# Kernel tuning notes

Hardware: AMD Instinct MI355X
Metric: run time of the kernel (lower is better)

Reference implementation:

```python
import jax, jax.numpy as jnp
import numpy as np

N_NODES = 46080   # 512 graphs x 90 nodes
NPG = 90          # nodes per graph (AAL atlas)
G = 512           # number of graphs
E = 737280        # edges (degree 16)
IN_DIM = 90
H = 64            # hidden_channels
K = 70            # sort-pool k


def setup_inputs() -> dict:
    key = jax.random.key(0)
    ks = jax.random.split(key, 12)
    x = jax.random.normal(ks[0], (N_NODES, IN_DIM), dtype=jnp.float32)
    # intra-graph random edges: src/dst within each graph's 90-node block
    gidx = jnp.repeat(jnp.arange(G, dtype=jnp.int64), E // G) * NPG
    src = jax.random.randint(ks[1], (E,), 0, NPG, dtype=jnp.int64) + gidx
    dst = jax.random.randint(ks[2], (E,), 0, NPG, dtype=jnp.int64) + gidx
    edge_index = jnp.stack([src, dst])
    edge_weight = jax.random.uniform(ks[3], (E,), dtype=jnp.float32)
    batch = jnp.repeat(jnp.arange(G, dtype=jnp.int64), NPG)
    s1 = 1.0 / np.sqrt(IN_DIM)
    s2 = 1.0 / np.sqrt(H)
    sk = 1.0 / np.sqrt(H * K)
    W1 = jax.random.uniform(ks[4], (IN_DIM, H), jnp.float32, -s1, s1)
    b1 = jnp.zeros((H,), jnp.float32)
    W2 = jax.random.uniform(ks[5], (H, H), jnp.float32, -s2, s2)
    b2 = jnp.zeros((H,), jnp.float32)
    lw1 = jax.random.uniform(ks[6], (H * K, H), jnp.float32, -sk, sk)
    lb1 = jax.random.uniform(ks[7], (H,), jnp.float32, -sk, sk)
    lw2 = jax.random.uniform(ks[8], (H, 1), jnp.float32, -s2, s2)
    lb2 = jax.random.uniform(ks[9], (1,), jnp.float32, -s2, s2)
    return {"x": x, "edge_index": edge_index, "edge_weight": edge_weight,
            "batch": batch, "W1": W1, "b1": b1, "W2": W2, "b2": b2,
            "lw1": lw1, "lb1": lb1, "lw2": lw2, "lb2": lb2}


def _gcn_conv(x, W, b, src, dst, ew, n):
    # PyG GCNConv: add self-loops (weight 1), symmetric normalization,
    # message = norm * (x @ W)[src], scatter-add to dst, add bias.
    xw = x @ W
    loop = jnp.arange(n)
    src_f = jnp.concatenate([src, loop])
    dst_f = jnp.concatenate([dst, loop])
    ew_f = jnp.concatenate([ew, jnp.ones((n,), x.dtype)])
    deg = jax.ops.segment_sum(ew_f, dst_f, num_segments=n)
    dinv = jnp.where(deg > 0, jax.lax.rsqrt(jnp.maximum(deg, 1e-12)), 0.0)
    norm = dinv[src_f] * ew_f * dinv[dst_f]
    msg = xw[src_f] * norm[:, None]          # [E+n, H] irregular gather
    out = jax.ops.segment_sum(msg, dst_f, num_segments=n)
    return out + b


def reference(x, edge_index, edge_weight, batch, W1, b1, W2, b2, lw1, lb1, lw2, lb2):
    src, dst = edge_index[0], edge_index[1]
    h1 = _gcn_conv(x, W1, b1, src, dst, edge_weight, N_NODES)
    x_train = h1
    h = jax.nn.relu(h1)
    h2 = _gcn_conv(h, W2, b2, src, dst, edge_weight, N_NODES)
    # global_sort_pool: per graph, sort nodes descending by last channel, keep top K.
    # batch is contiguous with NPG nodes/graph, so a reshape is exact.
    hg = h2.reshape(G, NPG, H)
    order = jnp.argsort(-hg[:, :, -1], axis=1)          # [G, NPG] descending
    hs = jnp.take_along_axis(hg, order[:, :, None], axis=1)
    pooled = hs[:, :K, :].reshape(G, K * H)
    # F.dropout(p=0.5, training=False) -> identity at inference
    z = pooled @ lw1 + lb1
    z = z @ lw2 + lb2
    out = jax.nn.sigmoid(z).squeeze(-1)                  # [G]
    return out, x_train
```

## Files before the change

kernel.cpp:

```cpp
#include <hip/hip_runtime.h>


#define NG      512
#define NPG     90
#define EPG     1440
#define IN_DIM  90
#define HD      64
#define KP      70
#define E_TOT   (NG*EPG)

#define WEFF_OFF   0
#define EPACK_OFF  4608
#define RS_OFF     (EPACK_OFF + NG*EPG)
#define D2_OFF     (RS_OFF + NG*96)
#define HW2_OFF    (D2_OFF + NG*96)

__global__ __launch_bounds__(256) void k0_csr(
    const int* __restrict__ ei, const float* __restrict__ ew,
    const float* __restrict__ lw1, const float* __restrict__ lb1,
    const float* __restrict__ lw2, const float* __restrict__ lb2,
    float* __restrict__ ws)
{
    __shared__ float s_deg[NPG];
    __shared__ int   s_indeg[NPG];
    __shared__ int   s_rowstart[NPG+1];
    __shared__ int   s_cursor[NPG];

    const int g = blockIdx.x, t = threadIdx.x;
    const int ebase = g*EPG, nbase = g*NPG;

    if (t < NPG) { s_deg[t] = 1.0f; s_indeg[t] = 0; }
    __syncthreads();
    for (int e = t; e < EPG; e += 256) {
        int d = ei[E_TOT + ebase + e] - nbase;
        atomicAdd(&s_deg[d], ew[ebase + e]);
        atomicAdd(&s_indeg[d], 1);
    }
    __syncthreads();
    if (t < NPG) s_deg[t] = rsqrtf(fmaxf(s_deg[t], 1e-12f));
    if (t <= NPG) {
        int acc = 0;
        for (int i = 0; i < t; ++i) acc += s_indeg[i];
        s_rowstart[t] = acc;
        if (t < NPG) s_cursor[t] = acc;
    }
    __syncthreads();

    unsigned* epk = (unsigned*)ws + EPACK_OFF + g*EPG;
    for (int e = t; e < EPG; e += 256) {
        int s = ei[ebase + e] - nbase;
        int d = ei[E_TOT + ebase + e] - nbase;
        float nrm = s_deg[s] * ew[ebase + e] * s_deg[d];
        int pos = atomicAdd(&s_cursor[d], 1);
        epk[pos] = (__float_as_uint(nrm) & ~127u) | (unsigned)s;
    }
    if (t <= NPG) ((int*)ws)[RS_OFF + g*96 + t] = s_rowstart[t];
    if (t < NPG)  ws[D2_OFF + g*96 + t] = s_deg[t]*s_deg[t];

    int i = g*256 + t;
    if (g < 18) {
        if (i < KP*HD) {
            const float4* row = (const float4*)(lw1 + (size_t)i*HD);
            const float4* w   = (const float4*)lw2;
            float s = 0.f;
            #pragma unroll
            for (int j4 = 0; j4 < HD/4; ++j4) {
                float4 r = row[j4], v = w[j4];
                s += r.x*v.x + r.y*v.y + r.z*v.z + r.w*v.w;
            }
            ws[WEFF_OFF + i] = s;
        } else if (i == KP*HD) {
            float s = lb2[0];
            for (int jj = 0; jj < HD; ++jj) s += lb1[jj]*lw2[jj];
            ws[WEFF_OFF + KP*HD] = s;
        }
    }
}

__global__ __launch_bounds__(256) void k1_gemm1(
    const float* __restrict__ x, const float* __restrict__ W1,
    float* __restrict__ xw)
{
    __shared__ float sx[16*IN_DIM];
    const int t = threadIdx.x;
    const int row0 = blockIdx.x * 16;

    const float4* gx = (const float4*)(x + (size_t)row0*IN_DIM);
    for (int i = t; i < 16*IN_DIM/4; i += 256) ((float4*)sx)[i] = gx[i];
    __syncthreads();

    const int j = t & 63, rg = t >> 6;
    float a0 = 0.f, a1 = 0.f, a2 = 0.f, a3 = 0.f;
    const float2* xp0 = (const float2*)&sx[(rg*4+0)*IN_DIM];
    const float2* xp1 = (const float2*)&sx[(rg*4+1)*IN_DIM];
    const float2* xp2 = (const float2*)&sx[(rg*4+2)*IN_DIM];
    const float2* xp3 = (const float2*)&sx[(rg*4+3)*IN_DIM];
    #pragma unroll 9
    for (int kh = 0; kh < IN_DIM/2; ++kh) {
        float w0 = W1[(2*kh)*HD + j];
        float w1 = W1[(2*kh+1)*HD + j];
        float2 v0 = xp0[kh], v1 = xp1[kh], v2 = xp2[kh], v3 = xp3[kh];
        a0 += v0.x*w0 + v0.y*w1;
        a1 += v1.x*w0 + v1.y*w1;
        a2 += v2.x*w0 + v2.y*w1;
        a3 += v3.x*w0 + v3.y*w1;
    }
    float* o = xw + (size_t)(row0 + rg*4)*HD + j;
    o[0*HD] = a0; o[1*HD] = a1; o[2*HD] = a2; o[3*HD] = a3;
}

__global__ __launch_bounds__(256) void k2_scatter1(
    float* __restrict__ xt,
    const float* __restrict__ b1,
    const float* __restrict__ ws)
{
    __shared__ float    sxw[NPG*16];
    __shared__ unsigned sep[EPG];
    __shared__ int      srs[NPG+1];
    __shared__ float    sd2[NPG];

    const int t = threadIdx.x;
    const int g = blockIdx.x >> 2, q = blockIdx.x & 3;
    const int c0 = q*16, nbase = g*NPG;

    const unsigned* epk = (const unsigned*)ws + EPACK_OFF + g*EPG;
    for (int i = t; i < EPG; i += 256) sep[i] = epk[i];
    if (t <= NPG) srs[t] = ((const int*)ws)[RS_OFF + g*96 + t];
    if (t < NPG)  sd2[t] = ws[D2_OFF + g*96 + t];
    for (int i = t; i < NPG*4; i += 256) {
        int row = i >> 2, f = i & 3;
        ((float4*)sxw)[i] = *(const float4*)(xt + (size_t)(nbase+row)*HD + c0 + f*4);
    }
    __syncthreads();

    for (int o = t; o < NPG*16; o += 256) {
        int d = o >> 4, c = o & 15;
        float a = sd2[d]*sxw[o];
        int p0 = srs[d], p1 = srs[d+1];
        for (int p = p0; p < p1; ++p) {
            unsigned u = sep[p];
            a += __uint_as_float(u & ~127u) * sxw[(int)(u & 127u)*16 + c];
        }
        xt[(size_t)(nbase+d)*HD + c0 + c] = a + b1[c0+c];
    }
}

__global__ __launch_bounds__(256) void k3_gemm2(
    const float* __restrict__ xt, const float* __restrict__ W2,
    float* __restrict__ ws)
{
    __shared__ float sh[16*HD];
    const int t = threadIdx.x;
    const int row0 = blockIdx.x * 16;

    const float4* gh = (const float4*)(xt + (size_t)row0*HD);
    for (int i = t; i < 16*HD/4; i += 256) {
        float4 v = gh[i];
        v.x = fmaxf(v.x, 0.f); v.y = fmaxf(v.y, 0.f);
        v.z = fmaxf(v.z, 0.f); v.w = fmaxf(v.w, 0.f);
        ((float4*)sh)[i] = v;
    }
    __syncthreads();

    const int j = t & 63, rg = t >> 6;
    float a0 = 0.f, a1 = 0.f, a2 = 0.f, a3 = 0.f;
    #pragma unroll 4
    for (int k4 = 0; k4 < HD/4; ++k4) {
        int k = k4*4;
        float4 h0 = *(const float4*)&sh[(rg*4+0)*HD + k];
        float4 h1 = *(const float4*)&sh[(rg*4+1)*HD + k];
        float4 h2 = *(const float4*)&sh[(rg*4+2)*HD + k];
        float4 h3 = *(const float4*)&sh[(rg*4+3)*HD + k];
        float w0 = W2[(k+0)*HD + j];
        float w1 = W2[(k+1)*HD + j];
        float w2 = W2[(k+2)*HD + j];
        float w3 = W2[(k+3)*HD + j];
        a0 += h0.x*w0 + h0.y*w1 + h0.z*w2 + h0.w*w3;
        a1 += h1.x*w0 + h1.y*w1 + h1.z*w2 + h1.w*w3;
        a2 += h2.x*w0 + h2.y*w1 + h2.z*w2 + h2.w*w3;
        a3 += h3.x*w0 + h3.y*w1 + h3.z*w2 + h3.w*w3;
    }
    float* o = ws + HW2_OFF + (size_t)(row0 + rg*4)*HD + j;
    o[0*HD] = a0; o[1*HD] = a1; o[2*HD] = a2; o[3*HD] = a3;
}

__global__ __launch_bounds__(512) void k4_final(
    const float* __restrict__ b2,
    const float* __restrict__ ws,
    float* __restrict__ out)
{
    __shared__ float    sB[NPG*HD];
    __shared__ float    sC[NPG*HD];
    __shared__ unsigned sep[EPG];
    __shared__ int      srs[NPG+1];
    __shared__ float    sd2[NPG];
    __shared__ int      s_ranknode[KP];
    __shared__ float    s_red[8];

    const int g = blockIdx.x, t = threadIdx.x;
    const int j = t & 63, grp = t >> 6;
    const int nbase = g*NPG;

    const float4* gb = (const float4*)(ws + HW2_OFF + (size_t)nbase*HD);
    for (int i = t; i < NPG*HD/4; i += 512) ((float4*)sB)[i] = gb[i];
    const unsigned* epk = (const unsigned*)ws + EPACK_OFF + g*EPG;
    for (int i = t; i < EPG; i += 512) sep[i] = epk[i];
    if (t <= NPG) srs[t] = ((const int*)ws)[RS_OFF + g*96 + t];
    if (t < NPG)  sd2[t] = ws[D2_OFF + g*96 + t];
    __syncthreads();

    for (int o = t; o < NPG*HD; o += 512) {
        int d = o >> 6, c = o & 63;
        float a = sd2[d]*sB[o];
        int p0 = srs[d], p1 = srs[d+1];
        for (int p = p0; p < p1; ++p) {
            unsigned u = sep[p];
            a += __uint_as_float(u & ~127u) * sB[(int)(u & 127u)*HD + c];
        }
        sC[o] = a + b2[c];
    }
    __syncthreads();

    if (t < NPG) {
        float vi = sC[t*HD + (HD-1)];
        int rank = 0;
        for (int jj = 0; jj < NPG; ++jj) {
            float vj = sC[jj*HD + (HD-1)];
            rank += (vj > vi) || (vj == vi && jj < t);
        }
        if (rank < KP) s_ranknode[rank] = t;
    }
    __syncthreads();

    float part = 0.f;
    #pragma unroll
    for (int m = 0; m < 9; ++m) {
        int i = t + m*512;
        if (i < KP*HD) {
            int k = i >> 6, c = i & 63;
            part += ws[WEFF_OFF + i] * sC[s_ranknode[k]*HD + c];
        }
    }
    #pragma unroll
    for (int off = 32; off > 0; off >>= 1) part += __shfl_down(part, off, 64);
    if (j == 0) s_red[grp] = part;
    __syncthreads();
    if (t == 0) {
        float zz = ws[WEFF_OFF + KP*HD];
        #pragma unroll
        for (int m = 0; m < 8; ++m) zz += s_red[m];
        out[g] = 1.0f / (1.0f + expf(-zz));
    }
}

extern "C" void kernel_launch(void* const* d_in, const int* in_sizes, int n_in,
                              void* d_out, int out_size, void* d_ws, size_t ws_size,
                              hipStream_t stream) {
    const float* x   = (const float*)d_in[0];
    const int*   ei  = (const int*)  d_in[1];
    const float* ew  = (const float*)d_in[2];
    const float* W1  = (const float*)d_in[4];
    const float* b1  = (const float*)d_in[5];
    const float* W2  = (const float*)d_in[6];
    const float* b2  = (const float*)d_in[7];
    const float* lw1 = (const float*)d_in[8];
    const float* lb1 = (const float*)d_in[9];
    const float* lw2 = (const float*)d_in[10];
    const float* lb2 = (const float*)d_in[11];

    float* ws     = (float*)d_ws;
    float* out    = (float*)d_out;
    float* xtrain = out + NG;

    k0_csr    <<<NG,   256, 0, stream>>>(ei, ew, lw1, lb1, lw2, lb2, ws);
    k1_gemm1  <<<2880, 256, 0, stream>>>(x, W1, xtrain);
    k2_scatter1<<<NG*4, 256, 0, stream>>>(xtrain, b1, ws);
    k3_gemm2  <<<2880, 256, 0, stream>>>(xtrain, W2, ws);
    k4_final  <<<NG,   512, 0, stream>>>(b2, ws, out);
}
```

Baseline: 177.5 us.

## Merge independent stages into shared grids and split final aggregation across blocks

Merges the CSR build, weight precompute and first GEMM into one launch with block-index dispatch. The second GEMM now shares a launch with a new per-graph ranking stage, which computes only the last channel of the second convolution to sort nodes. With the ranking done up front, the final aggregation splits each graph across two 256-thread blocks over channel halves and combines them with an atomic add. A small sigmoid kernel finishes the output. The aims are to cut serialized launch gaps and raise occupancy in the last stage, at the cost of recomputing the sort channel, an extra launch, and float atomics whose summation order is nondeterministic.

```diff
diff --git a/kernel.cpp b/kernel.cpp
--- a/kernel.cpp
+++ b/kernel.cpp
@@ -14,51 +14,78 @@
 #define RS_OFF     (EPACK_OFF + NG*EPG)
 #define D2_OFF     (RS_OFF + NG*96)
 #define HW2_OFF    (D2_OFF + NG*96)
-
-__global__ __launch_bounds__(256) void k0_csr(
-    const int* __restrict__ ei, const float* __restrict__ ew,
+#define RANK_OFF   (HW2_OFF + 46080*HD)
+#define ZACC_OFF   (RANK_OFF + NG*72)
+
+__global__ __launch_bounds__(256) void k_pre(
+    const float* __restrict__ x, const int* __restrict__ ei,
+    const float* __restrict__ ew, const float* __restrict__ W1,
     const float* __restrict__ lw1, const float* __restrict__ lb1,
     const float* __restrict__ lw2, const float* __restrict__ lb2,
-    float* __restrict__ ws)
-{
+    float* __restrict__ ws, float* __restrict__ xt)
+{
+    __shared__ float sx[16*IN_DIM];
     __shared__ float s_deg[NPG];
     __shared__ int   s_indeg[NPG];
     __shared__ int   s_rowstart[NPG+1];
     __shared__ int   s_cursor[NPG];
 
-    const int g = blockIdx.x, t = threadIdx.x;
-    const int ebase = g*EPG, nbase = g*NPG;
-
-    if (t < NPG) { s_deg[t] = 1.0f; s_indeg[t] = 0; }
-    __syncthreads();
-    for (int e = t; e < EPG; e += 256) {
-        int d = ei[E_TOT + ebase + e] - nbase;
-        atomicAdd(&s_deg[d], ew[ebase + e]);
-        atomicAdd(&s_indeg[d], 1);
-    }
-    __syncthreads();
-    if (t < NPG) s_deg[t] = rsqrtf(fmaxf(s_deg[t], 1e-12f));
-    if (t <= NPG) {
-        int acc = 0;
-        for (int i = 0; i < t; ++i) acc += s_indeg[i];
-        s_rowstart[t] = acc;
-        if (t < NPG) s_cursor[t] = acc;
-    }
-    __syncthreads();
-
-    unsigned* epk = (unsigned*)ws + EPACK_OFF + g*EPG;
-    for (int e = t; e < EPG; e += 256) {
-        int s = ei[ebase + e] - nbase;
-        int d = ei[E_TOT + ebase + e] - nbase;
-        float nrm = s_deg[s] * ew[ebase + e] * s_deg[d];
-        int pos = atomicAdd(&s_cursor[d], 1);
-        epk[pos] = (__float_as_uint(nrm) & ~127u) | (unsigned)s;
-    }
-    if (t <= NPG) ((int*)ws)[RS_OFF + g*96 + t] = s_rowstart[t];
-    if (t < NPG)  ws[D2_OFF + g*96 + t] = s_deg[t]*s_deg[t];
-
-    int i = g*256 + t;
-    if (g < 18) {
+    const int b = blockIdx.x, t = threadIdx.x;
+
+    if (b < 2880) {
+        const int row0 = b*16;
+        const float4* gx = (const float4*)(x + (size_t)row0*IN_DIM);
+        for (int i = t; i < 16*IN_DIM/4; i += 256) ((float4*)sx)[i] = gx[i];
+        __syncthreads();
+        const int j = t & 63, rg = t >> 6;
+        const float2* xp0 = (const float2*)&sx[(rg*4+0)*IN_DIM];
+        const float2* xp1 = (const float2*)&sx[(rg*4+1)*IN_DIM];
+        const float2* xp2 = (const float2*)&sx[(rg*4+2)*IN_DIM];
+        const float2* xp3 = (const float2*)&sx[(rg*4+3)*IN_DIM];
+        float a0 = 0.f, a1 = 0.f, a2 = 0.f, a3 = 0.f;
+        #pragma unroll 9
+        for (int kh = 0; kh < IN_DIM/2; ++kh) {
+            float w0 = W1[(2*kh)*HD + j];
+            float w1 = W1[(2*kh+1)*HD + j];
+            float2 v0 = xp0[kh], v1 = xp1[kh], v2 = xp2[kh], v3 = xp3[kh];
+            a0 += v0.x*w0 + v0.y*w1;
+            a1 += v1.x*w0 + v1.y*w1;
+            a2 += v2.x*w0 + v2.y*w1;
+            a3 += v3.x*w0 + v3.y*w1;
+        }
+        float* o = xt + (size_t)(row0 + rg*4)*HD + j;
+        o[0*HD] = a0; o[1*HD] = a1; o[2*HD] = a2; o[3*HD] = a3;
+    } else if (b < 3392) {
+        const int g = b - 2880;
+        const int ebase = g*EPG, nbase = g*NPG;
+        if (t < NPG) { s_deg[t] = 1.0f; s_indeg[t] = 0; }
+        __syncthreads();
+        for (int e = t; e < EPG; e += 256) {
+            int d = ei[E_TOT + ebase + e] - nbase;
+            atomicAdd(&s_deg[d], ew[ebase + e]);
+            atomicAdd(&s_indeg[d], 1);
+        }
+        __syncthreads();
+        if (t < NPG) s_deg[t] = rsqrtf(fmaxf(s_deg[t], 1e-12f));
+        if (t <= NPG) {
+            int acc = 0;
+            for (int i = 0; i < t; ++i) acc += s_indeg[i];
+            s_rowstart[t] = acc;
+            if (t < NPG) s_cursor[t] = acc;
+        }
+        __syncthreads();
+        unsigned* epk = (unsigned*)ws + EPACK_OFF + g*EPG;
+        for (int e = t; e < EPG; e += 256) {
+            int s = ei[ebase + e] - nbase;
+            int d = ei[E_TOT + ebase + e] - nbase;
+            float nrm = s_deg[s] * ew[ebase + e] * s_deg[d];
+            int pos = atomicAdd(&s_cursor[d], 1);
+            epk[pos] = (__float_as_uint(nrm) & ~127u) | (unsigned)s;
+        }
+        if (t <= NPG) ((int*)ws)[RS_OFF + g*96 + t] = s_rowstart[t];
+        if (t < NPG)  ws[D2_OFF + g*96 + t] = s_deg[t]*s_deg[t];
+    } else {
+        int i = (b-3392)*256 + t;
         if (i < KP*HD) {
             const float4* row = (const float4*)(lw1 + (size_t)i*HD);
             const float4* w   = (const float4*)lw2;
@@ -77,180 +104,192 @@
     }
 }
 
-__global__ __launch_bounds__(256) void k1_gemm1(
-    const float* __restrict__ x, const float* __restrict__ W1,
-    float* __restrict__ xw)
-{
-    __shared__ float sx[16*IN_DIM];
-    const int t = threadIdx.x;
-    const int row0 = blockIdx.x * 16;
-
-    const float4* gx = (const float4*)(x + (size_t)row0*IN_DIM);
-    for (int i = t; i < 16*IN_DIM/4; i += 256) ((float4*)sx)[i] = gx[i];
-    __syncthreads();
-
-    const int j = t & 63, rg = t >> 6;
-    float a0 = 0.f, a1 = 0.f, a2 = 0.f, a3 = 0.f;
-    const float2* xp0 = (const float2*)&sx[(rg*4+0)*IN_DIM];
-    const float2* xp1 = (const float2*)&sx[(rg*4+1)*IN_DIM];
-    const float2* xp2 = (const float2*)&sx[(rg*4+2)*IN_DIM];
-    const float2* xp3 = (const float2*)&sx[(rg*4+3)*IN_DIM];
-    #pragma unroll 9
-    for (int kh = 0; kh < IN_DIM/2; ++kh) {
-        float w0 = W1[(2*kh)*HD + j];
-        float w1 = W1[(2*kh+1)*HD + j];
-        float2 v0 = xp0[kh], v1 = xp1[kh], v2 = xp2[kh], v3 = xp3[kh];
-        a0 += v0.x*w0 + v0.y*w1;
-        a1 += v1.x*w0 + v1.y*w1;
-        a2 += v2.x*w0 + v2.y*w1;
-        a3 += v3.x*w0 + v3.y*w1;
-    }
-    float* o = xw + (size_t)(row0 + rg*4)*HD + j;
-    o[0*HD] = a0; o[1*HD] = a1; o[2*HD] = a2; o[3*HD] = a3;
-}
-
-__global__ __launch_bounds__(256) void k2_scatter1(
-    float* __restrict__ xt,
-    const float* __restrict__ b1,
+__global__ __launch_bounds__(256) void k_sc1(
+    float* __restrict__ xt, const float* __restrict__ b1,
     const float* __restrict__ ws)
 {
-    __shared__ float    sxw[NPG*16];
+    __shared__ float    sxw[NPG*32];
     __shared__ unsigned sep[EPG];
     __shared__ int      srs[NPG+1];
     __shared__ float    sd2[NPG];
 
     const int t = threadIdx.x;
-    const int g = blockIdx.x >> 2, q = blockIdx.x & 3;
-    const int c0 = q*16, nbase = g*NPG;
+    const int g = blockIdx.x >> 1, c0 = (blockIdx.x & 1)*32;
+    const int nbase = g*NPG;
 
     const unsigned* epk = (const unsigned*)ws + EPACK_OFF + g*EPG;
     for (int i = t; i < EPG; i += 256) sep[i] = epk[i];
     if (t <= NPG) srs[t] = ((const int*)ws)[RS_OFF + g*96 + t];
     if (t < NPG)  sd2[t] = ws[D2_OFF + g*96 + t];
-    for (int i = t; i < NPG*4; i += 256) {
-        int row = i >> 2, f = i & 3;
+    for (int i = t; i < NPG*8; i += 256) {
+        int row = i >> 3, f = i & 7;
         ((float4*)sxw)[i] = *(const float4*)(xt + (size_t)(nbase+row)*HD + c0 + f*4);
     }
     __syncthreads();
 
-    for (int o = t; o < NPG*16; o += 256) {
-        int d = o >> 4, c = o & 15;
+    for (int o = t; o < NPG*32; o += 256) {
+        int d = o >> 5, c = o & 31;
         float a = sd2[d]*sxw[o];
         int p0 = srs[d], p1 = srs[d+1];
         for (int p = p0; p < p1; ++p) {
             unsigned u = sep[p];
-            a += __uint_as_float(u & ~127u) * sxw[(int)(u & 127u)*16 + c];
+            a += __uint_as_float(u & ~127u) * sxw[(int)(u & 127u)*32 + c];
         }
         xt[(size_t)(nbase+d)*HD + c0 + c] = a + b1[c0+c];
     }
 }
 
-__global__ __launch_bounds__(256) void k3_gemm2(
+__global__ __launch_bounds__(256) void k_g2rank(
     const float* __restrict__ xt, const float* __restrict__ W2,
-    float* __restrict__ ws)
-{
-    __shared__ float sh[16*HD];
-    const int t = threadIdx.x;
-    const int row0 = blockIdx.x * 16;
-
-    const float4* gh = (const float4*)(xt + (size_t)row0*HD);
-    for (int i = t; i < 16*HD/4; i += 256) {
-        float4 v = gh[i];
-        v.x = fmaxf(v.x, 0.f); v.y = fmaxf(v.y, 0.f);
-        v.z = fmaxf(v.z, 0.f); v.w = fmaxf(v.w, 0.f);
-        ((float4*)sh)[i] = v;
-    }
-    __syncthreads();
-
-    const int j = t & 63, rg = t >> 6;
-    float a0 = 0.f, a1 = 0.f, a2 = 0.f, a3 = 0.f;
-    #pragma unroll 4
-    for (int k4 = 0; k4 < HD/4; ++k4) {
-        int k = k4*4;
-        float4 h0 = *(const float4*)&sh[(rg*4+0)*HD + k];
-        float4 h1 = *(const float4*)&sh[(rg*4+1)*HD + k];
-        float4 h2 = *(const float4*)&sh[(rg*4+2)*HD + k];
-        float4 h3 = *(const float4*)&sh[(rg*4+3)*HD + k];
-        float w0 = W2[(k+0)*HD + j];
-        float w1 = W2[(k+1)*HD + j];
-        float w2 = W2[(k+2)*HD + j];
-        float w3 = W2[(k+3)*HD + j];
-        a0 += h0.x*w0 + h0.y*w1 + h0.z*w2 + h0.w*w3;
-        a1 += h1.x*w0 + h1.y*w1 + h1.z*w2 + h1.w*w3;
-        a2 += h2.x*w0 + h2.y*w1 + h2.z*w2 + h2.w*w3;
-        a3 += h3.x*w0 + h3.y*w1 + h3.z*w2 + h3.w*w3;
-    }
-    float* o = ws + HW2_OFF + (size_t)(row0 + rg*4)*HD + j;
-    o[0*HD] = a0; o[1*HD] = a1; o[2*HD] = a2; o[3*HD] = a3;
-}
-
-__global__ __launch_bounds__(512) void k4_final(
-    const float* __restrict__ b2,
-    const float* __restrict__ ws,
-    float* __restrict__ out)
-{
-    __shared__ float    sB[NPG*HD];
-    __shared__ float    sC[NPG*HD];
+    const float* __restrict__ b2, float* __restrict__ ws)
+{
+    __shared__ float    sh[16*HD];
+    __shared__ float    sw2c[HD];
+    __shared__ float    scol[NPG];
+    __shared__ float    h263[NPG];
     __shared__ unsigned sep[EPG];
     __shared__ int      srs[NPG+1];
     __shared__ float    sd2[NPG];
-    __shared__ int      s_ranknode[KP];
-    __shared__ float    s_red[8];
-
-    const int g = blockIdx.x, t = threadIdx.x;
+    __shared__ int      srank[KP];
+
+    const int b = blockIdx.x, t = threadIdx.x;
+
+    if (b < 2880) {
+        const int row0 = b*16;
+        const float4* gh = (const float4*)(xt + (size_t)row0*HD);
+        for (int i = t; i < 16*HD/4; i += 256) {
+            float4 v = gh[i];
+            v.x = fmaxf(v.x, 0.f); v.y = fmaxf(v.y, 0.f);
+            v.z = fmaxf(v.z, 0.f); v.w = fmaxf(v.w, 0.f);
+            ((float4*)sh)[i] = v;
+        }
+        __syncthreads();
+        const int j = t & 63, rg = t >> 6;
+        float a0 = 0.f, a1 = 0.f, a2 = 0.f, a3 = 0.f;
+        #pragma unroll 4
+        for (int k4 = 0; k4 < HD/4; ++k4) {
+            int k = k4*4;
+            float4 h0 = *(const float4*)&sh[(rg*4+0)*HD + k];
+            float4 h1 = *(const float4*)&sh[(rg*4+1)*HD + k];
+            float4 h2 = *(const float4*)&sh[(rg*4+2)*HD + k];
+            float4 h3 = *(const float4*)&sh[(rg*4+3)*HD + k];
+            float w0 = W2[(k+0)*HD + j];
+            float w1 = W2[(k+1)*HD + j];
+            float w2 = W2[(k+2)*HD + j];
+            float w3 = W2[(k+3)*HD + j];
+            a0 += h0.x*w0 + h0.y*w1 + h0.z*w2 + h0.w*w3;
+            a1 += h1.x*w0 + h1.y*w1 + h1.z*w2 + h1.w*w3;
+            a2 += h2.x*w0 + h2.y*w1 + h2.z*w2 + h2.w*w3;
+            a3 += h3.x*w0 + h3.y*w1 + h3.z*w2 + h3.w*w3;
+        }
+        float* o = ws + HW2_OFF + (size_t)(row0 + rg*4)*HD + j;
+        o[0*HD] = a0; o[1*HD] = a1; o[2*HD] = a2; o[3*HD] = a3;
+    } else {
+        const int g = b - 2880;
+        const int nbase = g*NPG;
+        if (t < HD) sw2c[t] = W2[t*HD + 63];
+        const unsigned* epk = (const unsigned*)ws + EPACK_OFF + g*EPG;
+        for (int i = t; i < EPG; i += 256) sep[i] = epk[i];
+        if (t <= NPG) srs[t] = ((const int*)ws)[RS_OFF + g*96 + t];
+        if (t < NPG)  sd2[t] = ws[D2_OFF + g*96 + t];
+        __syncthreads();
+        if (t < NPG*4) {
+            int n = t >> 2, q = t & 3;
+            const float* row = xt + (size_t)(nbase+n)*HD + q*16;
+            float s = 0.f;
+            #pragma unroll
+            for (int k = 0; k < 16; ++k) s += fmaxf(row[k], 0.f)*sw2c[q*16+k];
+            s += __shfl_down(s, 2, 4);
+            s += __shfl_down(s, 1, 4);
+            if (q == 0) scol[n] = s;
+        }
+        __syncthreads();
+        if (t < NPG) {
+            float a = sd2[t]*scol[t];
+            int p0 = srs[t], p1 = srs[t+1];
+            for (int p = p0; p < p1; ++p) {
+                unsigned u = sep[p];
+                a += __uint_as_float(u & ~127u) * scol[(int)(u & 127u)];
+            }
+            h263[t] = a + b2[63];
+        }
+        __syncthreads();
+        if (t < NPG) {
+            float vi = h263[t];
+            int rank = 0;
+            for (int jj = 0; jj < NPG; ++jj) {
+                float vj = h263[jj];
+                rank += (vj > vi) || (vj == vi && jj < t);
+            }
+            if (rank < KP) srank[rank] = t;
+        }
+        if (t == 255) ws[ZACC_OFF + g] = 0.f;
+        __syncthreads();
+        if (t < KP) ((int*)ws)[RANK_OFF + g*72 + t] = srank[t];
+    }
+}
+
+__global__ __launch_bounds__(256) void k_fin(
+    const float* __restrict__ b2, float* __restrict__ ws)
+{
+    __shared__ float    sBh[NPG*32];
+    __shared__ float    sCh[NPG*32];
+    __shared__ unsigned sep[EPG];
+    __shared__ int      srs[NPG+1];
+    __shared__ float    sd2[NPG];
+    __shared__ int      srank[KP];
+    __shared__ float    sred[4];
+
+    const int t = threadIdx.x;
+    const int g = blockIdx.x >> 1, c0 = (blockIdx.x & 1)*32;
+    const int nbase = g*NPG;
     const int j = t & 63, grp = t >> 6;
-    const int nbase = g*NPG;
-
-    const float4* gb = (const float4*)(ws + HW2_OFF + (size_t)nbase*HD);
-    for (int i = t; i < NPG*HD/4; i += 512) ((float4*)sB)[i] = gb[i];
+
+    for (int i = t; i < NPG*8; i += 256) {
+        int row = i >> 3, f = i & 7;
+        ((float4*)sBh)[i] = *(const float4*)(ws + HW2_OFF + (size_t)(nbase+row)*HD + c0 + f*4);
+    }
     const unsigned* epk = (const unsigned*)ws + EPACK_OFF + g*EPG;
-    for (int i = t; i < EPG; i += 512) sep[i] = epk[i];
+    for (int i = t; i < EPG; i += 256) sep[i] = epk[i];
     if (t <= NPG) srs[t] = ((const int*)ws)[RS_OFF + g*96 + t];
     if (t < NPG)  sd2[t] = ws[D2_OFF + g*96 + t];
+    if (t < KP)   srank[t] = ((const int*)ws)[RANK_OFF + g*72 + t];
     __syncthreads();
 
-    for (int o = t; o < NPG*HD; o += 512) {
-        int d = o >> 6, c = o & 63;
-        float a = sd2[d]*sB[o];
+    for (int o = t; o < NPG*32; o += 256) {
+        int d = o >> 5, c = o & 31;
+        float a = sd2[d]*sBh[o];
         int p0 = srs[d], p1 = srs[d+1];
         for (int p = p0; p < p1; ++p) {
             unsigned u = sep[p];
-            a += __uint_as_float(u & ~127u) * sB[(int)(u & 127u)*HD + c];
-        }
-        sC[o] = a + b2[c];
-    }
-    __syncthreads();
-
-    if (t < NPG) {
-        float vi = sC[t*HD + (HD-1)];
-        int rank = 0;
-        for (int jj = 0; jj < NPG; ++jj) {
-            float vj = sC[jj*HD + (HD-1)];
-            rank += (vj > vi) || (vj == vi && jj < t);
-        }
-        if (rank < KP) s_ranknode[rank] = t;
+            a += __uint_as_float(u & ~127u) * sBh[(int)(u & 127u)*32 + c];
+        }
+        sCh[o] = a + b2[c0+c];
     }
     __syncthreads();
 
     float part = 0.f;
     #pragma unroll
     for (int m = 0; m < 9; ++m) {
-        int i = t + m*512;
-        if (i < KP*HD) {
-            int k = i >> 6, c = i & 63;
-            part += ws[WEFF_OFF + i] * sC[s_ranknode[k]*HD + c];
+        int i = t + m*256;
+        if (i < KP*32) {
+            int k = i >> 5, c = i & 31;
+            part += ws[WEFF_OFF + k*HD + c0 + c] * sCh[srank[k]*32 + c];
         }
     }
     #pragma unroll
     for (int off = 32; off > 0; off >>= 1) part += __shfl_down(part, off, 64);
-    if (j == 0) s_red[grp] = part;
+    if (j == 0) sred[grp] = part;
     __syncthreads();
-    if (t == 0) {
-        float zz = ws[WEFF_OFF + KP*HD];
-        #pragma unroll
-        for (int m = 0; m < 8; ++m) zz += s_red[m];
-        out[g] = 1.0f / (1.0f + expf(-zz));
-    }
+    if (t == 0) atomicAdd(&ws[ZACC_OFF + g], sred[0]+sred[1]+sred[2]+sred[3]);
+}
+
+__global__ __launch_bounds__(256) void k_sig(
+    const float* __restrict__ ws, float* __restrict__ out)
+{
+    int i = blockIdx.x*256 + threadIdx.x;
+    if (i < NG)
+        out[i] = 1.0f / (1.0f + expf(-(ws[ZACC_OFF + i] + ws[WEFF_OFF + KP*HD])));
 }
 
 extern "C" void kernel_launch(void* const* d_in, const int* in_sizes, int n_in,
@@ -272,9 +311,9 @@
     float* out    = (float*)d_out;
     float* xtrain = out + NG;
 
-    k0_csr    <<<NG,   256, 0, stream>>>(ei, ew, lw1, lb1, lw2, lb2, ws);
-    k1_gemm1  <<<2880, 256, 0, stream>>>(x, W1, xtrain);
-    k2_scatter1<<<NG*4, 256, 0, stream>>>(xtrain, b1, ws);
-    k3_gemm2  <<<2880, 256, 0, stream>>>(xtrain, W2, ws);
-    k4_final  <<<NG,   512, 0, stream>>>(b2, ws, out);
-}
+    k_pre   <<<3410, 256, 0, stream>>>(x, ei, ew, W1, lw1, lb1, lw2, lb2, ws, xtrain);
+    k_sc1   <<<1024, 256, 0, stream>>>(xtrain, b1, ws);
+    k_g2rank<<<3392, 256, 0, stream>>>(xtrain, W2, b2, ws);
+    k_fin   <<<1024, 256, 0, stream>>>(b2, ws);
+    k_sig   <<<2,    256, 0, stream>>>(ws, out);
+}
```

After: 181.7 us. 1.02x slower.

## Fuse five kernels into two: merged preprocessing and per-graph fused GCN pipeline

Applied to the files above, without the earlier changes.

Merges the CSR build, first GEMM and the weight-folding precompute into one heterogeneous launch dispatched by block index. A second per-graph kernel now does the layer-1 scatter, ReLU, the layer-2 GEMM in shared memory, the layer-2 scatter, the sort-pool and the head. This removes three launches and the global round trips for the intermediate h and hw2 tensors. In exchange the layer-1 scatter and GEMM2 run with only 512 blocks instead of thousands, which lowers parallelism, and the large LDS footprint may limit occupancy.

```diff
diff --git a/kernel.cpp b/kernel.cpp
--- a/kernel.cpp
+++ b/kernel.cpp
@@ -13,52 +13,76 @@
 #define EPACK_OFF  4608
 #define RS_OFF     (EPACK_OFF + NG*EPG)
 #define D2_OFF     (RS_OFF + NG*96)
-#define HW2_OFF    (D2_OFF + NG*96)
-
-__global__ __launch_bounds__(256) void k0_csr(
-    const int* __restrict__ ei, const float* __restrict__ ew,
+
+__global__ __launch_bounds__(256) void k_pre(
+    const float* __restrict__ x, const int* __restrict__ ei,
+    const float* __restrict__ ew, const float* __restrict__ W1,
     const float* __restrict__ lw1, const float* __restrict__ lb1,
     const float* __restrict__ lw2, const float* __restrict__ lb2,
-    float* __restrict__ ws)
+    float* __restrict__ ws, float* __restrict__ xt)
 {
+    __shared__ float sx[16*IN_DIM];
     __shared__ float s_deg[NPG];
     __shared__ int   s_indeg[NPG];
     __shared__ int   s_rowstart[NPG+1];
     __shared__ int   s_cursor[NPG];
 
-    const int g = blockIdx.x, t = threadIdx.x;
-    const int ebase = g*EPG, nbase = g*NPG;
-
-    if (t < NPG) { s_deg[t] = 1.0f; s_indeg[t] = 0; }
-    __syncthreads();
-    for (int e = t; e < EPG; e += 256) {
-        int d = ei[E_TOT + ebase + e] - nbase;
-        atomicAdd(&s_deg[d], ew[ebase + e]);
-        atomicAdd(&s_indeg[d], 1);
-    }
-    __syncthreads();
-    if (t < NPG) s_deg[t] = rsqrtf(fmaxf(s_deg[t], 1e-12f));
-    if (t <= NPG) {
-        int acc = 0;
-        for (int i = 0; i < t; ++i) acc += s_indeg[i];
-        s_rowstart[t] = acc;
-        if (t < NPG) s_cursor[t] = acc;
-    }
-    __syncthreads();
-
-    unsigned* epk = (unsigned*)ws + EPACK_OFF + g*EPG;
-    for (int e = t; e < EPG; e += 256) {
-        int s = ei[ebase + e] - nbase;
-        int d = ei[E_TOT + ebase + e] - nbase;
-        float nrm = s_deg[s] * ew[ebase + e] * s_deg[d];
-        int pos = atomicAdd(&s_cursor[d], 1);
-        epk[pos] = (__float_as_uint(nrm) & ~127u) | (unsigned)s;
-    }
-    if (t <= NPG) ((int*)ws)[RS_OFF + g*96 + t] = s_rowstart[t];
-    if (t < NPG)  ws[D2_OFF + g*96 + t] = s_deg[t]*s_deg[t];
-
-    int i = g*256 + t;
-    if (g < 18) {
+    const int b = blockIdx.x, t = threadIdx.x;
+
+    if (b < 2880) {
+        const int row0 = b*16;
+        const float4* gx = (const float4*)(x + (size_t)row0*IN_DIM);
+        for (int i = t; i < 16*IN_DIM/4; i += 256) ((float4*)sx)[i] = gx[i];
+        __syncthreads();
+        const int j = t & 63, rg = t >> 6;
+        const float2* xp0 = (const float2*)&sx[(rg*4+0)*IN_DIM];
+        const float2* xp1 = (const float2*)&sx[(rg*4+1)*IN_DIM];
+        const float2* xp2 = (const float2*)&sx[(rg*4+2)*IN_DIM];
+        const float2* xp3 = (const float2*)&sx[(rg*4+3)*IN_DIM];
+        float a0 = 0.f, a1 = 0.f, a2 = 0.f, a3 = 0.f;
+        #pragma unroll 9
+        for (int kh = 0; kh < IN_DIM/2; ++kh) {
+            float w0 = W1[(2*kh)*HD + j];
+            float w1 = W1[(2*kh+1)*HD + j];
+            float2 v0 = xp0[kh], v1 = xp1[kh], v2 = xp2[kh], v3 = xp3[kh];
+            a0 += v0.x*w0 + v0.y*w1;
+            a1 += v1.x*w0 + v1.y*w1;
+            a2 += v2.x*w0 + v2.y*w1;
+            a3 += v3.x*w0 + v3.y*w1;
+        }
+        float* o = xt + (size_t)(row0 + rg*4)*HD + j;
+        o[0*HD] = a0; o[1*HD] = a1; o[2*HD] = a2; o[3*HD] = a3;
+    } else if (b < 3392) {
+        const int g = b - 2880;
+        const int ebase = g*EPG, nbase = g*NPG;
+        if (t < NPG) { s_deg[t] = 1.0f; s_indeg[t] = 0; }
+        __syncthreads();
+        for (int e = t; e < EPG; e += 256) {
+            int d = ei[E_TOT + ebase + e] - nbase;
+            atomicAdd(&s_deg[d], ew[ebase + e]);
+            atomicAdd(&s_indeg[d], 1);
+        }
+        __syncthreads();
+        if (t < NPG) s_deg[t] = rsqrtf(fmaxf(s_deg[t], 1e-12f));
+        if (t <= NPG) {
+            int acc = 0;
+            for (int i = 0; i < t; ++i) acc += s_indeg[i];
+            s_rowstart[t] = acc;
+            if (t < NPG) s_cursor[t] = acc;
+        }
+        __syncthreads();
+        unsigned* epk = (unsigned*)ws + EPACK_OFF + g*EPG;
+        for (int e = t; e < EPG; e += 256) {
+            int s = ei[ebase + e] - nbase;
+            int d = ei[E_TOT + ebase + e] - nbase;
+            float nrm = s_deg[s] * ew[ebase + e] * s_deg[d];
+            int pos = atomicAdd(&s_cursor[d], 1);
+            epk[pos] = (__float_as_uint(nrm) & ~127u) | (unsigned)s;
+        }
+        if (t <= NPG) ((int*)ws)[RS_OFF + g*96 + t] = s_rowstart[t];
+        if (t < NPG)  ws[D2_OFF + g*96 + t] = s_deg[t]*s_deg[t];
+    } else {
+        int i = (b-3392)*256 + t;
         if (i < KP*HD) {
             const float4* row = (const float4*)(lw1 + (size_t)i*HD);
             const float4* w   = (const float4*)lw2;
@@ -77,138 +101,32 @@
     }
 }
 
-__global__ __launch_bounds__(256) void k1_gemm1(
-    const float* __restrict__ x, const float* __restrict__ W1,
-    float* __restrict__ xw)
-{
-    __shared__ float sx[16*IN_DIM];
-    const int t = threadIdx.x;
-    const int row0 = blockIdx.x * 16;
-
-    const float4* gx = (const float4*)(x + (size_t)row0*IN_DIM);
-    for (int i = t; i < 16*IN_DIM/4; i += 256) ((float4*)sx)[i] = gx[i];
-    __syncthreads();
-
-    const int j = t & 63, rg = t >> 6;
-    float a0 = 0.f, a1 = 0.f, a2 = 0.f, a3 = 0.f;
-    const float2* xp0 = (const float2*)&sx[(rg*4+0)*IN_DIM];
-    const float2* xp1 = (const float2*)&sx[(rg*4+1)*IN_DIM];
-    const float2* xp2 = (const float2*)&sx[(rg*4+2)*IN_DIM];
-    const float2* xp3 = (const float2*)&sx[(rg*4+3)*IN_DIM];
-    #pragma unroll 9
-    for (int kh = 0; kh < IN_DIM/2; ++kh) {
-        float w0 = W1[(2*kh)*HD + j];
-        float w1 = W1[(2*kh+1)*HD + j];
-        float2 v0 = xp0[kh], v1 = xp1[kh], v2 = xp2[kh], v3 = xp3[kh];
-        a0 += v0.x*w0 + v0.y*w1;
-        a1 += v1.x*w0 + v1.y*w1;
-        a2 += v2.x*w0 + v2.y*w1;
-        a3 += v3.x*w0 + v3.y*w1;
-    }
-    float* o = xw + (size_t)(row0 + rg*4)*HD + j;
-    o[0*HD] = a0; o[1*HD] = a1; o[2*HD] = a2; o[3*HD] = a3;
-}
-
-__global__ __launch_bounds__(256) void k2_scatter1(
-    float* __restrict__ xt,
-    const float* __restrict__ b1,
-    const float* __restrict__ ws)
-{
-    __shared__ float    sxw[NPG*16];
-    __shared__ unsigned sep[EPG];
-    __shared__ int      srs[NPG+1];
-    __shared__ float    sd2[NPG];
-
-    const int t = threadIdx.x;
-    const int g = blockIdx.x >> 2, q = blockIdx.x & 3;
-    const int c0 = q*16, nbase = g*NPG;
-
-    const unsigned* epk = (const unsigned*)ws + EPACK_OFF + g*EPG;
-    for (int i = t; i < EPG; i += 256) sep[i] = epk[i];
-    if (t <= NPG) srs[t] = ((const int*)ws)[RS_OFF + g*96 + t];
-    if (t < NPG)  sd2[t] = ws[D2_OFF + g*96 + t];
-    for (int i = t; i < NPG*4; i += 256) {
-        int row = i >> 2, f = i & 3;
-        ((float4*)sxw)[i] = *(const float4*)(xt + (size_t)(nbase+row)*HD + c0 + f*4);
-    }
-    __syncthreads();
-
-    for (int o = t; o < NPG*16; o += 256) {
-        int d = o >> 4, c = o & 15;
-        float a = sd2[d]*sxw[o];
-        int p0 = srs[d], p1 = srs[d+1];
-        for (int p = p0; p < p1; ++p) {
-            unsigned u = sep[p];
-            a += __uint_as_float(u & ~127u) * sxw[(int)(u & 127u)*16 + c];
-        }
-        xt[(size_t)(nbase+d)*HD + c0 + c] = a + b1[c0+c];
-    }
-}
-
-__global__ __launch_bounds__(256) void k3_gemm2(
-    const float* __restrict__ xt, const float* __restrict__ W2,
-    float* __restrict__ ws)
-{
-    __shared__ float sh[16*HD];
-    const int t = threadIdx.x;
-    const int row0 = blockIdx.x * 16;
-
-    const float4* gh = (const float4*)(xt + (size_t)row0*HD);
-    for (int i = t; i < 16*HD/4; i += 256) {
-        float4 v = gh[i];
-        v.x = fmaxf(v.x, 0.f); v.y = fmaxf(v.y, 0.f);
-        v.z = fmaxf(v.z, 0.f); v.w = fmaxf(v.w, 0.f);
-        ((float4*)sh)[i] = v;
-    }
-    __syncthreads();
-
-    const int j = t & 63, rg = t >> 6;
-    float a0 = 0.f, a1 = 0.f, a2 = 0.f, a3 = 0.f;
-    #pragma unroll 4
-    for (int k4 = 0; k4 < HD/4; ++k4) {
-        int k = k4*4;
-        float4 h0 = *(const float4*)&sh[(rg*4+0)*HD + k];
-        float4 h1 = *(const float4*)&sh[(rg*4+1)*HD + k];
-        float4 h2 = *(const float4*)&sh[(rg*4+2)*HD + k];
-        float4 h3 = *(const float4*)&sh[(rg*4+3)*HD + k];
-        float w0 = W2[(k+0)*HD + j];
-        float w1 = W2[(k+1)*HD + j];
-        float w2 = W2[(k+2)*HD + j];
-        float w3 = W2[(k+3)*HD + j];
-        a0 += h0.x*w0 + h0.y*w1 + h0.z*w2 + h0.w*w3;
-        a1 += h1.x*w0 + h1.y*w1 + h1.z*w2 + h1.w*w3;
-        a2 += h2.x*w0 + h2.y*w1 + h2.z*w2 + h2.w*w3;
-        a3 += h3.x*w0 + h3.y*w1 + h3.z*w2 + h3.w*w3;
-    }
-    float* o = ws + HW2_OFF + (size_t)(row0 + rg*4)*HD + j;
-    o[0*HD] = a0; o[1*HD] = a1; o[2*HD] = a2; o[3*HD] = a3;
-}
-
-__global__ __launch_bounds__(512) void k4_final(
-    const float* __restrict__ b2,
-    const float* __restrict__ ws,
-    float* __restrict__ out)
+__global__ __launch_bounds__(512, 4) void k_graph(
+    const float* __restrict__ b1, const float* __restrict__ W2,
+    const float* __restrict__ b2, const float* __restrict__ ws,
+    float* __restrict__ out, float* __restrict__ xt)
 {
     __shared__ float    sB[NPG*HD];
     __shared__ float    sC[NPG*HD];
     __shared__ unsigned sep[EPG];
     __shared__ int      srs[NPG+1];
     __shared__ float    sd2[NPG];
-    __shared__ int      s_ranknode[KP];
-    __shared__ float    s_red[8];
+    __shared__ int      srank[KP];
+    __shared__ float    sred[8];
 
     const int g = blockIdx.x, t = threadIdx.x;
     const int j = t & 63, grp = t >> 6;
     const int nbase = g*NPG;
 
-    const float4* gb = (const float4*)(ws + HW2_OFF + (size_t)nbase*HD);
-    for (int i = t; i < NPG*HD/4; i += 512) ((float4*)sB)[i] = gb[i];
+    const float4* gxw = (const float4*)(xt + (size_t)nbase*HD);
+    for (int i = t; i < NPG*HD/4; i += 512) ((float4*)sB)[i] = gxw[i];
     const unsigned* epk = (const unsigned*)ws + EPACK_OFF + g*EPG;
     for (int i = t; i < EPG; i += 512) sep[i] = epk[i];
     if (t <= NPG) srs[t] = ((const int*)ws)[RS_OFF + g*96 + t];
     if (t < NPG)  sd2[t] = ws[D2_OFF + g*96 + t];
     __syncthreads();
 
+    float* xtg = xt + (size_t)nbase*HD;
     for (int o = t; o < NPG*HD; o += 512) {
         int d = o >> 6, c = o & 63;
         float a = sd2[d]*sB[o];
@@ -217,6 +135,49 @@
             unsigned u = sep[p];
             a += __uint_as_float(u & ~127u) * sB[(int)(u & 127u)*HD + c];
         }
+        a += b1[c];
+        xtg[o] = a;
+        sC[o] = fmaxf(a, 0.f);
+    }
+    __syncthreads();
+
+    for (int it = 0; it < 3; ++it) {
+        int r0 = it*32 + grp*4;
+        int rr0 = min(r0+0, NPG-1), rr1 = min(r0+1, NPG-1);
+        int rr2 = min(r0+2, NPG-1), rr3 = min(r0+3, NPG-1);
+        float a0 = 0.f, a1 = 0.f, a2 = 0.f, a3 = 0.f;
+        #pragma unroll 4
+        for (int k4 = 0; k4 < HD/4; ++k4) {
+            int k = k4*4;
+            float4 h0 = *(const float4*)&sC[rr0*HD + k];
+            float4 h1 = *(const float4*)&sC[rr1*HD + k];
+            float4 h2 = *(const float4*)&sC[rr2*HD + k];
+            float4 h3 = *(const float4*)&sC[rr3*HD + k];
+            float w0 = W2[(k+0)*HD + j];
+            float w1 = W2[(k+1)*HD + j];
+            float w2 = W2[(k+2)*HD + j];
+            float w3 = W2[(k+3)*HD + j];
+            a0 += h0.x*w0 + h0.y*w1 + h0.z*w2 + h0.w*w3;
+            a1 += h1.x*w0 + h1.y*w1 + h1.z*w2 + h1.w*w3;
+            a2 += h2.x*w0 + h2.y*w1 + h2.z*w2 + h2.w*w3;
+            a3 += h3.x*w0 + h3.y*w1 + h3.z*w2 + h3.w*w3;
+        }
+        __syncthreads();
+        if (r0+0 < NPG) sB[(r0+0)*HD + j] = a0;
+        if (r0+1 < NPG) sB[(r0+1)*HD + j] = a1;
+        if (r0+2 < NPG) sB[(r0+2)*HD + j] = a2;
+        if (r0+3 < NPG) sB[(r0+3)*HD + j] = a3;
+    }
+    __syncthreads();
+
+    for (int o = t; o < NPG*HD; o += 512) {
+        int d = o >> 6, c = o & 63;
+        float a = sd2[d]*sB[o];
+        int p0 = srs[d], p1 = srs[d+1];
+        for (int p = p0; p < p1; ++p) {
+            unsigned u = sep[p];
+            a += __uint_as_float(u & ~127u) * sB[(int)(u & 127u)*HD + c];
+        }
         sC[o] = a + b2[c];
     }
     __syncthreads();
@@ -228,7 +189,7 @@
             float vj = sC[jj*HD + (HD-1)];
             rank += (vj > vi) || (vj == vi && jj < t);
         }
-        if (rank < KP) s_ranknode[rank] = t;
+        if (rank < KP) srank[rank] = t;
     }
     __syncthreads();
 
@@ -238,17 +199,17 @@
         int i = t + m*512;
         if (i < KP*HD) {
             int k = i >> 6, c = i & 63;
-            part += ws[WEFF_OFF + i] * sC[s_ranknode[k]*HD + c];
+            part += ws[WEFF_OFF + i] * sC[srank[k]*HD + c];
         }
     }
     #pragma unroll
     for (int off = 32; off > 0; off >>= 1) part += __shfl_down(part, off, 64);
-    if (j == 0) s_red[grp] = part;
+    if (j == 0) sred[grp] = part;
     __syncthreads();
     if (t == 0) {
         float zz = ws[WEFF_OFF + KP*HD];
         #pragma unroll
-        for (int m = 0; m < 8; ++m) zz += s_red[m];
+        for (int m = 0; m < 8; ++m) zz += sred[m];
         out[g] = 1.0f / (1.0f + expf(-zz));
     }
 }
@@ -272,9 +233,6 @@
     float* out    = (float*)d_out;
     float* xtrain = out + NG;
 
-    k0_csr    <<<NG,   256, 0, stream>>>(ei, ew, lw1, lb1, lw2, lb2, ws);
-    k1_gemm1  <<<2880, 256, 0, stream>>>(x, W1, xtrain);
-    k2_scatter1<<<NG*4, 256, 0, stream>>>(xtrain, b1, ws);
-    k3_gemm2  <<<2880, 256, 0, stream>>>(xtrain, W2, ws);
-    k4_final  <<<NG,   512, 0, stream>>>(b2, ws, out);
+    k_pre  <<<3410, 256, 0, stream>>>(x, ei, ew, W1, lw1, lb1, lw2, lb2, ws, xtrain);
+    k_graph<<<NG,   512, 0, stream>>>(b1, W2, b2, ws, out, xtrain);
 }
```

Measured after the change: 167.0 us. -5.9%, faster.
